# Kernel tuning notes

Measured on AMD Instinct MI355X. Metric: run time of the kernel, lower is better.

Reference implementation:

```python
import jax, jax.numpy as jnp
import numpy as np

B = 1024       # repertoires (batch)
TCR = 100      # instances (TCRs) per repertoire
FEAT = 15      # feature_num (conv in_channels)
AA = 24        # aa_num (sequence length)
KS = [2, 3, 4, 5, 6, 7]
FN = [3, 3, 3, 2, 2, 1]
NINP = 14      # sum(FN)
EPS = 1e-5     # BatchNorm eps


def sparsemax(z):
    # z: (B, K); sparsemax along axis 1 (Martins & Astudillo 2016)
    K = z.shape[1]
    zs = -jnp.sort(-z, axis=1)               # descending sort
    cs = jnp.cumsum(zs, axis=1)
    k = jnp.arange(1, K + 1, dtype=z.dtype)
    support = 1.0 + k * zs > cs              # (B, K) bool
    ksel = jnp.sum(support, axis=1, keepdims=True).astype(jnp.int32)  # support size
    tau = (jnp.take_along_axis(cs, ksel - 1, axis=1) - 1.0) / ksel.astype(z.dtype)
    return jnp.maximum(z - tau, 0.0)


def setup_inputs() -> dict:
    key = jax.random.key(0)
    ks = jax.random.split(key, 12)
    inp = {"x": jax.random.normal(ks[0], (B, TCR, FEAT, AA), dtype=jnp.float32)}
    for i, (h, f) in enumerate(zip(KS, FN)):
        inp[f"cw{i}"] = jax.random.normal(ks[1 + i], (f, FEAT, h), dtype=jnp.float32) * 0.1
        inp[f"cb{i}"] = jnp.zeros((f,), dtype=jnp.float32)
    inp["fc1_w"] = jax.random.normal(ks[7], (NINP, NINP), dtype=jnp.float32) * 0.2
    inp["fc1_b"] = jnp.zeros((NINP,), dtype=jnp.float32)
    inp["waout_w"] = jax.random.normal(ks[8], (1, NINP), dtype=jnp.float32) * 0.2
    inp["decf_w"] = jax.random.normal(ks[9], (NINP, NINP), dtype=jnp.float32) * 0.2
    inp["decf_b"] = jnp.zeros((NINP,), dtype=jnp.float32)
    inp["bn_g"] = jnp.ones((NINP,), dtype=jnp.float32)
    inp["bn_b"] = jnp.zeros((NINP,), dtype=jnp.float32)
    inp["decs_w"] = jax.random.normal(ks[10], (2, NINP), dtype=jnp.float32) * 0.2
    inp["decs_b"] = jnp.zeros((2,), dtype=jnp.float32)
    return inp


def reference(x, cw0, cb0, cw1, cb1, cw2, cb2, cw3, cb3, cw4, cb4, cw5, cb5,
              fc1_w, fc1_b, waout_w, decf_w, decf_b, bn_g, bn_b, decs_w, decs_b):
    xf = x.reshape(-1, FEAT, AA)  # (B*TCR, 15, 24)
    feats = []
    for w, b in ((cw0, cb0), (cw1, cb1), (cw2, cb2), (cw3, cb3), (cw4, cb4), (cw5, cb5)):
        y = jax.lax.conv_general_dilated(xf, w, (1,), 'VALID',
                                         dimension_numbers=('NCH', 'OIH', 'NCH'))
        y = jax.nn.relu(y + b[None, :, None])
        feats.append(jnp.max(y, axis=-1))  # AdaptiveMaxPool1d(1): global max over length
    out = jnp.concatenate(feats, axis=1).reshape(-1, TCR, NINP)  # (B, TCR, 14)
    # fclayer1 + dropout(eval=identity) + relu; applied per-instance so the
    # torch (TCR, B, .) transpose is equivalent to working in (B, TCR, .)
    h = jax.nn.relu(out @ fc1_w.T + fc1_b)                       # (B, TCR, 14)
    attw = sparsemax(h @ waout_w[0])                             # (B, TCR)
    pooled = jnp.einsum('bt,btd->bd', attw, h)                   # bmm(attw[:,None,:], h)
    z = pooled @ decf_w.T + decf_b                               # decoder_f
    mu = jnp.mean(z, axis=0)                                     # BatchNorm1d (batch stats)
    var = jnp.var(z, axis=0)
    z = jax.nn.relu((z - mu) / jnp.sqrt(var + EPS) * bn_g + bn_b)
    logits = z @ decs_w.T + decs_b                               # decoder_s -> (B, 2)
    return logits, attw
```

## Files before the change

### kernel.cpp

```cpp
#include <hip/hip_runtime.h>

typedef unsigned int  u32;
typedef unsigned short u16;

__device__ __forceinline__ float bf2f(u16 u){
    return __uint_as_float(((u32)u) << 16);
}
__device__ __forceinline__ float lo16(u32 v){ return __uint_as_float(v << 16); }
__device__ __forceinline__ float hi16(u32 v){ return __uint_as_float(v & 0xffff0000u); }
__device__ __forceinline__ u16 f2bf(float f){
    u32 x = __float_as_uint(f);
    x += 0x7fffu + ((x >> 16) & 1u);
    return (u16)(x >> 16);
}
__device__ __forceinline__ float ldany(const void* p, int i, bool bf){
    return bf ? bf2f(((const u16*)p)[i]) : ((const float*)p)[i];
}

#define B_      1024
#define TCR_    100
#define NINST   (B_*TCR_)

#define OFF_WCH    0
#define OFF_CB     840
#define OFF_FC1W   854
#define OFF_FC1B   1050
#define OFF_WA     1064
#define OFF_DECFW  1078
#define OFF_DECFB  1274
#define OFF_BNG    1288
#define OFF_BNB    1302
#define OFF_DECSW  1316
#define OFF_DECSB  1344

__global__ __launch_bounds__(256) void k_pack(
    const void* cw0, const void* cb0, const void* cw1, const void* cb1,
    const void* cw2, const void* cb2, const void* cw3, const void* cb3,
    const void* cw4, const void* cb4, const void* cw5, const void* cb5,
    const void* fc1_w, const void* fc1_b, const void* waout,
    const void* decf_w, const void* decf_b,
    const void* bn_g, const void* bn_b,
    const void* decs_w, const void* decs_b,
    float* __restrict__ wsP)
{
    const int tid = threadIdx.x;
    const bool bf = (((const u16*)bn_g)[0] == 0x3F80u);

    for (int widx = tid; widx < 840; widx += 256){
        float val; int dst;
        if (widx < 90)      { int e = widx;       int c=e/6,  rr=e-c*6,  ff=rr/2, j=rr-ff*2; val=ldany(cw0,(ff*15+c)*2+j,bf); dst=c*56+ 0+ff*2+j; }
        else if (widx < 225){ int e = widx - 90;  int c=e/9,  rr=e-c*9,  ff=rr/3, j=rr-ff*3; val=ldany(cw1,(ff*15+c)*3+j,bf); dst=c*56+ 6+ff*3+j; }
        else if (widx < 405){ int e = widx - 225; int c=e/12, rr=e-c*12, ff=rr/4, j=rr-ff*4; val=ldany(cw2,(ff*15+c)*4+j,bf); dst=c*56+15+ff*4+j; }
        else if (widx < 555){ int e = widx - 405; int c=e/10, rr=e-c*10, ff=rr/5, j=rr-ff*5; val=ldany(cw3,(ff*15+c)*5+j,bf); dst=c*56+27+ff*5+j; }
        else if (widx < 735){ int e = widx - 555; int c=e/12, rr=e-c*12, ff=rr/6, j=rr-ff*6; val=ldany(cw4,(ff*15+c)*6+j,bf); dst=c*56+37+ff*6+j; }
        else                { int e = widx - 735; int c=e/7,  j=e-c*7;                        val=ldany(cw5,c*7+j,bf);        dst=c*56+49+j; }
        wsP[OFF_WCH + dst] = val;
    }
    for (int i = tid; i < 14; i += 256){
        float bv;
        if (i < 3)       bv = ldany(cb0, i, bf);
        else if (i < 6)  bv = ldany(cb1, i - 3, bf);
        else if (i < 9)  bv = ldany(cb2, i - 6, bf);
        else if (i < 11) bv = ldany(cb3, i - 9, bf);
        else if (i < 13) bv = ldany(cb4, i - 11, bf);
        else             bv = ldany(cb5, 0, bf);
        wsP[OFF_CB    + i] = bv;
        wsP[OFF_FC1B  + i] = ldany(fc1_b,  i, bf);
        wsP[OFF_WA    + i] = ldany(waout,  i, bf);
        wsP[OFF_DECFB + i] = ldany(decf_b, i, bf);
        wsP[OFF_BNG   + i] = ldany(bn_g,   i, bf);
        wsP[OFF_BNB   + i] = ldany(bn_b,   i, bf);
    }
    for (int i = tid; i < 196; i += 256){
        wsP[OFF_FC1W  + i] = ldany(fc1_w,  i, bf);
        wsP[OFF_DECFW + i] = ldany(decf_w, i, bf);
    }
    for (int i = tid; i < 28; i += 256) wsP[OFF_DECSW + i] = ldany(decs_w, i, bf);
    for (int i = tid; i < 2;  i += 256) wsP[OFF_DECSB + i] = ldany(decs_b, i, bf);
}

template<int H, int F, int GOFF>
__device__ __forceinline__ void acc_ch(float (&acc)[F][17 - H], const float* xr,
                                       const float* __restrict__ wch){
    float wv[F * H];
    #pragma unroll
    for (int k = 0; k < F * H; ++k) wv[k] = wch[GOFF + k];
    #pragma unroll
    for (int ff = 0; ff < F; ++ff)
        #pragma unroll
        for (int i = 0; i < 17 - H; ++i)
            #pragma unroll
            for (int j = 0; j < H; ++j)
                acc[ff][i] = fmaf(wv[ff * H + j], xr[i + j], acc[ff][i]);
}

template<int H, int F, int OF>
__device__ __forceinline__ void pair_max(float (&acc)[F][17 - H],
                                         const float* __restrict__ wsP, float* feats){
    #pragma unroll
    for (int ff = 0; ff < F; ++ff){
        float m = acc[ff][0];
        #pragma unroll
        for (int i = 1; i < 17 - H; ++i) m = fmaxf(m, acc[ff][i]);
        m = fmaxf(m, __shfl_xor(m, 1));
        feats[OF + ff] = fmaxf(m + wsP[OFF_CB + OF + ff], 0.0f);
    }
}

template<bool BF>
__device__ __forceinline__ void unpack16(const uint4* buf, float* xr){
    if (BF){
        #pragma unroll
        for (int i = 0; i < 2; ++i){
            u32 w0 = buf[i].x, w1 = buf[i].y, w2 = buf[i].z, w3 = buf[i].w;
            xr[i*8+0] = lo16(w0); xr[i*8+1] = hi16(w0);
            xr[i*8+2] = lo16(w1); xr[i*8+3] = hi16(w1);
            xr[i*8+4] = lo16(w2); xr[i*8+5] = hi16(w2);
            xr[i*8+6] = lo16(w3); xr[i*8+7] = hi16(w3);
        }
    } else {
        #pragma unroll
        for (int i = 0; i < 4; ++i){
            xr[i*4+0] = __uint_as_float(buf[i].x);
            xr[i*4+1] = __uint_as_float(buf[i].y);
            xr[i*4+2] = __uint_as_float(buf[i].z);
            xr[i*4+3] = __uint_as_float(buf[i].w);
        }
    }
}

template<bool BF>
__device__ __forceinline__ void conv_body(const void* __restrict__ x,
                                          const float* __restrict__ wsP,
                                          float* __restrict__ hbufT,
                                          float* __restrict__ sbuf){
    constexpr int NB = BF ? 2 : 4;
    constexpr int CS = BF ? 48 : 96;
    const int tid   = threadIdx.x;
    const int tpart = tid & 1;
    const int inst  = blockIdx.x * 128 + (tid >> 1);
    const char* xb  = (const char*)x + (size_t)inst * (BF ? 720 : 1440)
                                     + tpart * (BF ? 16 : 32);

    float a2[3][15], a3[3][14], a4[3][13], a5[2][12], a6[2][11], a7[1][10];
    #pragma unroll
    for (int f = 0; f < 3; ++f){
        #pragma unroll
        for (int i = 0; i < 15; ++i) a2[f][i] = 0.0f;
        #pragma unroll
        for (int i = 0; i < 14; ++i) a3[f][i] = 0.0f;
        #pragma unroll
        for (int i = 0; i < 13; ++i) a4[f][i] = 0.0f;
    }
    #pragma unroll
    for (int f = 0; f < 2; ++f){
        #pragma unroll
        for (int i = 0; i < 12; ++i) a5[f][i] = 0.0f;
        #pragma unroll
        for (int i = 0; i < 11; ++i) a6[f][i] = 0.0f;
    }
    #pragma unroll
    for (int i = 0; i < 10; ++i) a7[0][i] = 0.0f;

    uint4 cur[NB];
    {
        const uint4* p = (const uint4*)xb;
        #pragma unroll
        for (int i = 0; i < NB; ++i) cur[i] = p[i];
    }
    #pragma unroll 1
    for (int c = 0; c < 15; ++c){
        uint4 nxt[NB];
        int cn = (c < 14) ? (c + 1) : 14;
        const uint4* pn = (const uint4*)(xb + cn * CS);
        #pragma unroll
        for (int i = 0; i < NB; ++i) nxt[i] = pn[i];

        float xr[16];
        unpack16<BF>(cur, xr);
        const float* wch = wsP + OFF_WCH + c * 56;
        acc_ch<2,3, 0>(a2, xr, wch);
        acc_ch<3,3, 6>(a3, xr, wch);
        acc_ch<4,3,15>(a4, xr, wch);
        acc_ch<5,2,27>(a5, xr, wch);
        acc_ch<6,2,37>(a6, xr, wch);
        acc_ch<7,1,49>(a7, xr, wch);

        #pragma unroll
        for (int i = 0; i < NB; ++i) cur[i] = nxt[i];
    }

    float feats[14];
    pair_max<2,3, 0>(a2, wsP, feats);
    pair_max<3,3, 3>(a3, wsP, feats);
    pair_max<4,3, 6>(a4, wsP, feats);
    pair_max<5,2, 9>(a5, wsP, feats);
    pair_max<6,2,11>(a6, wsP, feats);
    pair_max<7,1,13>(a7, wsP, feats);

    float hv[14];
    #pragma unroll
    for (int i = 0; i < 14; ++i){
        float a = wsP[OFF_FC1B + i];
        #pragma unroll
        for (int j = 0; j < 14; ++j) a = fmaf(feats[j], wsP[OFF_FC1W + i * 14 + j], a);
        hv[i] = fmaxf(a, 0.0f);
    }
    float sc = 0.0f;
    #pragma unroll
    for (int i = 0; i < 14; ++i) sc = fmaf(hv[i], wsP[OFF_WA + i], sc);

    if (tpart == 0){
        #pragma unroll
        for (int d = 0; d < 14; ++d) hbufT[d * NINST + inst] = hv[d];
        sbuf[inst] = sc;
    }
}

__global__ __launch_bounds__(256) void k_conv(
    const void* __restrict__ x, const float* __restrict__ wsP,
    const void* __restrict__ dt,
    float* __restrict__ hbufT, float* __restrict__ sbuf)
{
    const bool bf = (((const u16*)dt)[0] == 0x3F80u);
    if (bf) conv_body<true >(x, wsP, hbufT, sbuf);
    else    conv_body<false>(x, wsP, hbufT, sbuf);
}

__global__ __launch_bounds__(64) void k_sparse(
    const float* __restrict__ hbufT, const float* __restrict__ sbuf,
    const float* __restrict__ wsP, const void* __restrict__ dt,
    float* __restrict__ zbuf, void* __restrict__ d_out)
{
    const int b    = blockIdx.x;
    const int lane = threadIdx.x;
    const bool bf  = (((const u16*)dt)[0] == 0x3F80u);
    const bool has2 = lane < (TCR_ - 64);

    float z0 = sbuf[b * TCR_ + lane];
    float z1 = has2 ? sbuf[b * TCR_ + 64 + lane] : -1e30f;

    float m = fmaxf(z0, z1);
    #pragma unroll
    for (int o = 32; o; o >>= 1) m = fmaxf(m, __shfl_xor(m, o));

    float lo = m - 1.0f, hi = m;
    for (int it = 0; it < 32; ++it){
        float mid = 0.5f * (lo + hi);
        float s = fmaxf(z0 - mid, 0.0f) + fmaxf(z1 - mid, 0.0f);
        #pragma unroll
        for (int o = 32; o; o >>= 1) s += __shfl_xor(s, o);
        if (s >= 1.0f) lo = mid; else hi = mid;
    }
    float tau = 0.5f * (lo + hi);
    float a0 = fmaxf(z0 - tau, 0.0f);
    float a1 = fmaxf(z1 - tau, 0.0f);

    if (bf){
        u16* aw = (u16*)d_out + 2048;
        aw[b * TCR_ + lane] = f2bf(a0);
        if (has2) aw[b * TCR_ + 64 + lane] = f2bf(a1);
    } else {
        float* aw = (float*)d_out + 2048;
        aw[b * TCR_ + lane] = a0;
        if (has2) aw[b * TCR_ + 64 + lane] = a1;
    }

    float ap[14];
    #pragma unroll
    for (int d = 0; d < 14; ++d){
        float v = a0 * hbufT[d * NINST + b * TCR_ + lane];
        if (has2) v += a1 * hbufT[d * NINST + b * TCR_ + 64 + lane];
        #pragma unroll
        for (int o = 32; o; o >>= 1) v += __shfl_xor(v, o);
        ap[d] = v;
    }
    if (lane < 14){
        float zv = wsP[OFF_DECFB + lane];
        #pragma unroll
        for (int j = 0; j < 14; ++j) zv = fmaf(ap[j], wsP[OFF_DECFW + lane * 14 + j], zv);
        zbuf[b * 14 + lane] = zv;
    }
}

__global__ __launch_bounds__(256) void k_bn(
    const float* __restrict__ zbuf, const float* __restrict__ wsP,
    const void* __restrict__ dt, void* __restrict__ d_out)
{
    __shared__ float part[4][28];
    __shared__ float red[28];
    const int tid  = threadIdx.x;
    const int lane = tid & 63;
    const int w    = tid >> 6;
    const bool bf  = (((const u16*)dt)[0] == 0x3F80u);

    float z[4][14];
    #pragma unroll
    for (int r = 0; r < 4; ++r)
        #pragma unroll
        for (int d = 0; d < 14; ++d) z[r][d] = zbuf[(tid + 256 * r) * 14 + d];

    #pragma unroll
    for (int d = 0; d < 14; ++d){
        float s = 0.0f, q = 0.0f;
        #pragma unroll
        for (int r = 0; r < 4; ++r){ s += z[r][d]; q += z[r][d] * z[r][d]; }
        #pragma unroll
        for (int o = 32; o; o >>= 1){ s += __shfl_xor(s, o); q += __shfl_xor(q, o); }
        if (lane == 0){ part[w][d] = s; part[w][14 + d] = q; }
    }
    __syncthreads();
    if (tid < 28) red[tid] = part[0][tid] + part[1][tid] + part[2][tid] + part[3][tid];
    __syncthreads();

    float mu[14], rs[14];
    #pragma unroll
    for (int d = 0; d < 14; ++d){
        mu[d] = red[d] * (1.0f / 1024.0f);
        float var = red[14 + d] * (1.0f / 1024.0f) - mu[d] * mu[d];
        rs[d] = rsqrtf(var + 1e-5f);
    }
    #pragma unroll
    for (int r = 0; r < 4; ++r){
        float zn[14];
        #pragma unroll
        for (int d = 0; d < 14; ++d)
            zn[d] = fmaxf((z[r][d] - mu[d]) * rs[d] * wsP[OFF_BNG + d] + wsP[OFF_BNB + d], 0.0f);
        #pragma unroll
        for (int c = 0; c < 2; ++c){
            float a = wsP[OFF_DECSB + c];
            #pragma unroll
            for (int d = 0; d < 14; ++d) a = fmaf(zn[d], wsP[OFF_DECSW + c * 14 + d], a);
            if (bf) ((u16*)d_out)[(tid + 256 * r) * 2 + c] = f2bf(a);
            else    ((float*)d_out)[(tid + 256 * r) * 2 + c] = a;
        }
    }
}

extern "C" void kernel_launch(void* const* d_in, const int* in_sizes, int n_in,
                              void* d_out, int out_size, void* d_ws, size_t ws_size,
                              hipStream_t stream)
{
    (void)in_sizes; (void)n_in; (void)out_size; (void)ws_size;
    const void* x     = d_in[0];
    const void* bn_g  = d_in[18];

    float* wsP   = (float*)d_ws;
    float* hbufT = wsP + 2048;
    float* sbuf  = hbufT + (size_t)14 * NINST;
    float* zbuf  = sbuf + NINST;

    k_pack<<<1, 256, 0, stream>>>(
        d_in[1], d_in[2], d_in[3], d_in[4], d_in[5], d_in[6],
        d_in[7], d_in[8], d_in[9], d_in[10], d_in[11], d_in[12],
        d_in[13], d_in[14], d_in[15], d_in[16], d_in[17],
        d_in[18], d_in[19], d_in[20], d_in[21], wsP);
    k_conv<<<NINST / 128, 256, 0, stream>>>(x, wsP, bn_g, hbufT, sbuf);
    k_sparse<<<B_, 64, 0, stream>>>(hbufT, sbuf, wsP, bn_g, zbuf, d_out);
    k_bn<<<1, 256, 0, stream>>>(zbuf, wsP, bn_g, d_out);
}
```

Before: 298.3 us.

## Recast bf16 conv as Toeplitz MFMA GEMM and restructure fp32 conv per-lane

```diff
diff --git a/kernel.cpp b/kernel.cpp
--- a/kernel.cpp
+++ b/kernel.cpp
@@ -2,12 +2,12 @@
 
 typedef unsigned int  u32;
 typedef unsigned short u16;
+typedef __attribute__((ext_vector_type(8))) short short8;
+typedef __attribute__((ext_vector_type(4))) float f32x4;
 
 __device__ __forceinline__ float bf2f(u16 u){
     return __uint_as_float(((u32)u) << 16);
 }
-__device__ __forceinline__ float lo16(u32 v){ return __uint_as_float(v << 16); }
-__device__ __forceinline__ float hi16(u32 v){ return __uint_as_float(v & 0xffff0000u); }
 __device__ __forceinline__ u16 f2bf(float f){
     u32 x = __float_as_uint(f);
     x += 0x7fffu + ((x >> 16) & 1u);
@@ -20,6 +20,9 @@
 #define B_      1024
 #define TCR_    100
 #define NINST   (B_*TCR_)
+#define NT      21
+#define KS      12
+#define K2      384
 
 #define OFF_WCH    0
 #define OFF_CB     840
@@ -32,6 +35,7 @@
 #define OFF_BNB    1302
 #define OFF_DECSW  1316
 #define OFF_DECSB  1344
+#define OFF_HBUF   66560
 
 __global__ __launch_bounds__(256) void k_pack(
     const void* cw0, const void* cb0, const void* cw1, const void* cb1,
@@ -46,157 +50,177 @@
     const int tid = threadIdx.x;
     const bool bf = (((const u16*)bn_g)[0] == 0x3F80u);
 
-    for (int widx = tid; widx < 840; widx += 256){
-        float val; int dst;
-        if (widx < 90)      { int e = widx;       int c=e/6,  rr=e-c*6,  ff=rr/2, j=rr-ff*2; val=ldany(cw0,(ff*15+c)*2+j,bf); dst=c*56+ 0+ff*2+j; }
-        else if (widx < 225){ int e = widx - 90;  int c=e/9,  rr=e-c*9,  ff=rr/3, j=rr-ff*3; val=ldany(cw1,(ff*15+c)*3+j,bf); dst=c*56+ 6+ff*3+j; }
-        else if (widx < 405){ int e = widx - 225; int c=e/12, rr=e-c*12, ff=rr/4, j=rr-ff*4; val=ldany(cw2,(ff*15+c)*4+j,bf); dst=c*56+15+ff*4+j; }
-        else if (widx < 555){ int e = widx - 405; int c=e/10, rr=e-c*10, ff=rr/5, j=rr-ff*5; val=ldany(cw3,(ff*15+c)*5+j,bf); dst=c*56+27+ff*5+j; }
-        else if (widx < 735){ int e = widx - 555; int c=e/12, rr=e-c*12, ff=rr/6, j=rr-ff*6; val=ldany(cw4,(ff*15+c)*6+j,bf); dst=c*56+37+ff*6+j; }
-        else                { int e = widx - 735; int c=e/7,  j=e-c*7;                        val=ldany(cw5,c*7+j,bf);        dst=c*56+49+j; }
-        wsP[OFF_WCH + dst] = val;
-    }
-    for (int i = tid; i < 14; i += 256){
-        float bv;
-        if (i < 3)       bv = ldany(cb0, i, bf);
-        else if (i < 6)  bv = ldany(cb1, i - 3, bf);
-        else if (i < 9)  bv = ldany(cb2, i - 6, bf);
-        else if (i < 11) bv = ldany(cb3, i - 9, bf);
-        else if (i < 13) bv = ldany(cb4, i - 11, bf);
-        else             bv = ldany(cb5, 0, bf);
-        wsP[OFF_CB    + i] = bv;
-        wsP[OFF_FC1B  + i] = ldany(fc1_b,  i, bf);
-        wsP[OFF_WA    + i] = ldany(waout,  i, bf);
-        wsP[OFF_DECFB + i] = ldany(decf_b, i, bf);
-        wsP[OFF_BNG   + i] = ldany(bn_g,   i, bf);
-        wsP[OFF_BNB   + i] = ldany(bn_b,   i, bf);
-    }
-    for (int i = tid; i < 196; i += 256){
-        wsP[OFF_FC1W  + i] = ldany(fc1_w,  i, bf);
-        wsP[OFF_DECFW + i] = ldany(decf_w, i, bf);
-    }
-    for (int i = tid; i < 28; i += 256) wsP[OFF_DECSW + i] = ldany(decs_w, i, bf);
-    for (int i = tid; i < 2;  i += 256) wsP[OFF_DECSB + i] = ldany(decs_b, i, bf);
-}
-
-template<int H, int F, int GOFF>
-__device__ __forceinline__ void acc_ch(float (&acc)[F][17 - H], const float* xr,
-                                       const float* __restrict__ wch){
-    float wv[F * H];
-    #pragma unroll
-    for (int k = 0; k < F * H; ++k) wv[k] = wch[GOFF + k];
+    if (blockIdx.x == 0){
+        for (int widx = tid; widx < 840; widx += 256){
+            float val; int dst;
+            if (widx < 90)      { int e = widx;       int c=e/6,  rr=e-c*6,  ff=rr/2, j=rr-ff*2; val=ldany(cw0,(ff*15+c)*2+j,bf); dst=c*56+ 0+ff*2+j; }
+            else if (widx < 225){ int e = widx - 90;  int c=e/9,  rr=e-c*9,  ff=rr/3, j=rr-ff*3; val=ldany(cw1,(ff*15+c)*3+j,bf); dst=c*56+ 6+ff*3+j; }
+            else if (widx < 405){ int e = widx - 225; int c=e/12, rr=e-c*12, ff=rr/4, j=rr-ff*4; val=ldany(cw2,(ff*15+c)*4+j,bf); dst=c*56+15+ff*4+j; }
+            else if (widx < 555){ int e = widx - 405; int c=e/10, rr=e-c*10, ff=rr/5, j=rr-ff*5; val=ldany(cw3,(ff*15+c)*5+j,bf); dst=c*56+27+ff*5+j; }
+            else if (widx < 735){ int e = widx - 555; int c=e/12, rr=e-c*12, ff=rr/6, j=rr-ff*6; val=ldany(cw4,(ff*15+c)*6+j,bf); dst=c*56+37+ff*6+j; }
+            else                { int e = widx - 735; int c=e/7,  j=e-c*7;                        val=ldany(cw5,c*7+j,bf);        dst=c*56+49+j; }
+            wsP[OFF_WCH + dst] = val;
+        }
+        for (int i = tid; i < 14; i += 256){
+            float bv;
+            if (i < 3)       bv = ldany(cb0, i, bf);
+            else if (i < 6)  bv = ldany(cb1, i - 3, bf);
+            else if (i < 9)  bv = ldany(cb2, i - 6, bf);
+            else if (i < 11) bv = ldany(cb3, i - 9, bf);
+            else if (i < 13) bv = ldany(cb4, i - 11, bf);
+            else             bv = ldany(cb5, 0, bf);
+            wsP[OFF_CB    + i] = bv;
+            wsP[OFF_FC1B  + i] = ldany(fc1_b,  i, bf);
+            wsP[OFF_WA    + i] = ldany(waout,  i, bf);
+            wsP[OFF_DECFB + i] = ldany(decf_b, i, bf);
+            wsP[OFF_BNG   + i] = ldany(bn_g,   i, bf);
+            wsP[OFF_BNB   + i] = ldany(bn_b,   i, bf);
+        }
+        for (int i = tid; i < 196; i += 256){
+            wsP[OFF_FC1W  + i] = ldany(fc1_w,  i, bf);
+            wsP[OFF_DECFW + i] = ldany(decf_w, i, bf);
+        }
+        for (int i = tid; i < 28; i += 256) wsP[OFF_DECSW + i] = ldany(decs_w, i, bf);
+        for (int i = tid; i < 2;  i += 256) wsP[OFF_DECSB + i] = ldany(decs_b, i, bf);
+    }
+
+    u16* wt = (u16*)(wsP + 2048);
+    const int gstride = gridDim.x * 256;
+    for (int i = blockIdx.x * 256 + tid; i < 336 * K2; i += gstride){
+        int n = i / K2, k = i - n * K2;
+        int gff = n / 24, t = n - gff * 24;
+        int H = 2 + (gff>=3) + (gff>=6) + (gff>=9) + (gff>=11) + (gff>=13);
+        int limit = 25 - H;
+        float val = 0.0f;
+        if (k < 360 && t < limit){
+            int c = k / 24, u = k - c * 24;
+            int j = u - t;
+            if (j >= 0 && j < H){
+                if (gff < 3)       val = ldany(cw0, ((gff  )*15+c)*2+j, bf);
+                else if (gff < 6)  val = ldany(cw1, ((gff-3)*15+c)*3+j, bf);
+                else if (gff < 9)  val = ldany(cw2, ((gff-6)*15+c)*4+j, bf);
+                else if (gff < 11) val = ldany(cw3, ((gff-9)*15+c)*5+j, bf);
+                else if (gff < 13) val = ldany(cw4, ((gff-11)*15+c)*6+j, bf);
+                else               val = ldany(cw5, (c)*7+j, bf);
+            }
+        }
+        wt[(size_t)n * K2 + k] = f2bf(val);
+    }
+}
+
+template<int H, int F, int GOFF, int OF>
+__device__ __forceinline__ void f32_group(const float* __restrict__ xrow,
+                                          const float* __restrict__ wsP,
+                                          float* feats){
+    float acc[F][25 - H];
     #pragma unroll
     for (int ff = 0; ff < F; ++ff)
         #pragma unroll
-        for (int i = 0; i < 17 - H; ++i)
-            #pragma unroll
-            for (int j = 0; j < H; ++j)
-                acc[ff][i] = fmaf(wv[ff * H + j], xr[i + j], acc[ff][i]);
-}
-
-template<int H, int F, int OF>
-__device__ __forceinline__ void pair_max(float (&acc)[F][17 - H],
-                                         const float* __restrict__ wsP, float* feats){
+        for (int t = 0; t < 25 - H; ++t) acc[ff][t] = 0.0f;
+    for (int c = 0; c < 15; ++c){
+        float xr[24];
+        const float4* p = (const float4*)(xrow + c * 24);
+        #pragma unroll
+        for (int i = 0; i < 6; ++i){
+            float4 v = p[i];
+            xr[i*4+0] = v.x; xr[i*4+1] = v.y; xr[i*4+2] = v.z; xr[i*4+3] = v.w;
+        }
+        const float* wc = wsP + OFF_WCH + c * 56 + GOFF;
+        #pragma unroll
+        for (int ff = 0; ff < F; ++ff)
+            #pragma unroll
+            for (int t = 0; t < 25 - H; ++t)
+                #pragma unroll
+                for (int j = 0; j < H; ++j)
+                    acc[ff][t] = fmaf(wc[ff * H + j], xr[t + j], acc[ff][t]);
+    }
     #pragma unroll
     for (int ff = 0; ff < F; ++ff){
         float m = acc[ff][0];
         #pragma unroll
-        for (int i = 1; i < 17 - H; ++i) m = fmaxf(m, acc[ff][i]);
-        m = fmaxf(m, __shfl_xor(m, 1));
-        feats[OF + ff] = fmaxf(m + wsP[OFF_CB + OF + ff], 0.0f);
-    }
-}
-
-template<bool BF>
-__device__ __forceinline__ void unpack16(const uint4* buf, float* xr){
-    if (BF){
-        #pragma unroll
-        for (int i = 0; i < 2; ++i){
-            u32 w0 = buf[i].x, w1 = buf[i].y, w2 = buf[i].z, w3 = buf[i].w;
-            xr[i*8+0] = lo16(w0); xr[i*8+1] = hi16(w0);
-            xr[i*8+2] = lo16(w1); xr[i*8+3] = hi16(w1);
-            xr[i*8+4] = lo16(w2); xr[i*8+5] = hi16(w2);
-            xr[i*8+6] = lo16(w3); xr[i*8+7] = hi16(w3);
+        for (int t = 1; t < 25 - H; ++t) m = fmaxf(m, acc[ff][t]);
+        feats[OF + ff] = m;
+    }
+}
+
+__global__ __launch_bounds__(64, 2) void k_conv(
+    const void* __restrict__ x, const float* __restrict__ wsP,
+    const u16* __restrict__ wt, const void* __restrict__ dt,
+    float* __restrict__ hbufT, float* __restrict__ sbuf)
+{
+    __shared__ float pool[64][43];
+    const int lane = threadIdx.x;
+    const bool bf  = (((const u16*)dt)[0] == 0x3F80u);
+    const int instbase = blockIdx.x * 64;
+
+    float feats[14];
+
+    if (bf){
+        const int col  = lane & 15;
+        const int quad = lane >> 4;
+
+        short8 A[4][KS];
+        #pragma unroll
+        for (int ms = 0; ms < 4; ++ms){
+            const u16* xrow = (const u16*)x + (size_t)(instbase + ms * 16 + col) * 360;
+            #pragma unroll
+            for (int ks = 0; ks < KS; ++ks){
+                int k0 = ks * 32 + quad * 8;
+                if (k0 >= 360) k0 = 0;
+                A[ms][ks] = *(const short8*)(xrow + k0);
+            }
+        }
+
+        #pragma unroll 1
+        for (int nt = 0; nt < NT; ++nt){
+            f32x4 C[4];
+            #pragma unroll
+            for (int ms = 0; ms < 4; ++ms) C[ms] = (f32x4){0.f, 0.f, 0.f, 0.f};
+
+            const u16* wrow = wt + (size_t)(nt * 16 + col) * K2 + quad * 8;
+            #pragma unroll
+            for (int ks = 0; ks < KS; ++ks){
+                short8 Bf = *(const short8*)(wrow + ks * 32);
+                #pragma unroll
+                for (int ms = 0; ms < 4; ++ms)
+                    C[ms] = __builtin_amdgcn_mfma_f32_16x16x32_bf16(A[ms][ks], Bf, C[ms], 0, 0, 0);
+            }
+
+            int n = nt * 16 + col;
+            int g = (n * 2731) >> 16;
+            int pos = n - g * 24;
+            int limit = 23 - (g>=3) - (g>=6) - (g>=9) - (g>=11) - (g>=13);
+            bool valid = pos < limit;
+            int h = nt * 2 + (col >> 3);
+            #pragma unroll
+            for (int ms = 0; ms < 4; ++ms)
+                #pragma unroll
+                for (int r = 0; r < 4; ++r){
+                    float v = valid ? C[ms][r] : -3.0e38f;
+                    v = fmaxf(v, __shfl_xor(v, 1));
+                    v = fmaxf(v, __shfl_xor(v, 2));
+                    v = fmaxf(v, __shfl_xor(v, 4));
+                    if ((col & 7) == 0)
+                        pool[ms * 16 + quad * 4 + r][h] = v;
+                }
+        }
+        #pragma unroll
+        for (int g = 0; g < 14; ++g){
+            float m = fmaxf(fmaxf(pool[lane][3*g], pool[lane][3*g+1]), pool[lane][3*g+2]);
+            feats[g] = fmaxf(m + wsP[OFF_CB + g], 0.0f);
         }
     } else {
-        #pragma unroll
-        for (int i = 0; i < 4; ++i){
-            xr[i*4+0] = __uint_as_float(buf[i].x);
-            xr[i*4+1] = __uint_as_float(buf[i].y);
-            xr[i*4+2] = __uint_as_float(buf[i].z);
-            xr[i*4+3] = __uint_as_float(buf[i].w);
-        }
-    }
-}
-
-template<bool BF>
-__device__ __forceinline__ void conv_body(const void* __restrict__ x,
-                                          const float* __restrict__ wsP,
-                                          float* __restrict__ hbufT,
-                                          float* __restrict__ sbuf){
-    constexpr int NB = BF ? 2 : 4;
-    constexpr int CS = BF ? 48 : 96;
-    const int tid   = threadIdx.x;
-    const int tpart = tid & 1;
-    const int inst  = blockIdx.x * 128 + (tid >> 1);
-    const char* xb  = (const char*)x + (size_t)inst * (BF ? 720 : 1440)
-                                     + tpart * (BF ? 16 : 32);
-
-    float a2[3][15], a3[3][14], a4[3][13], a5[2][12], a6[2][11], a7[1][10];
-    #pragma unroll
-    for (int f = 0; f < 3; ++f){
-        #pragma unroll
-        for (int i = 0; i < 15; ++i) a2[f][i] = 0.0f;
-        #pragma unroll
-        for (int i = 0; i < 14; ++i) a3[f][i] = 0.0f;
-        #pragma unroll
-        for (int i = 0; i < 13; ++i) a4[f][i] = 0.0f;
-    }
-    #pragma unroll
-    for (int f = 0; f < 2; ++f){
-        #pragma unroll
-        for (int i = 0; i < 12; ++i) a5[f][i] = 0.0f;
-        #pragma unroll
-        for (int i = 0; i < 11; ++i) a6[f][i] = 0.0f;
-    }
-    #pragma unroll
-    for (int i = 0; i < 10; ++i) a7[0][i] = 0.0f;
-
-    uint4 cur[NB];
-    {
-        const uint4* p = (const uint4*)xb;
-        #pragma unroll
-        for (int i = 0; i < NB; ++i) cur[i] = p[i];
-    }
-    #pragma unroll 1
-    for (int c = 0; c < 15; ++c){
-        uint4 nxt[NB];
-        int cn = (c < 14) ? (c + 1) : 14;
-        const uint4* pn = (const uint4*)(xb + cn * CS);
-        #pragma unroll
-        for (int i = 0; i < NB; ++i) nxt[i] = pn[i];
-
-        float xr[16];
-        unpack16<BF>(cur, xr);
-        const float* wch = wsP + OFF_WCH + c * 56;
-        acc_ch<2,3, 0>(a2, xr, wch);
-        acc_ch<3,3, 6>(a3, xr, wch);
-        acc_ch<4,3,15>(a4, xr, wch);
-        acc_ch<5,2,27>(a5, xr, wch);
-        acc_ch<6,2,37>(a6, xr, wch);
-        acc_ch<7,1,49>(a7, xr, wch);
-
-        #pragma unroll
-        for (int i = 0; i < NB; ++i) cur[i] = nxt[i];
-    }
-
-    float feats[14];
-    pair_max<2,3, 0>(a2, wsP, feats);
-    pair_max<3,3, 3>(a3, wsP, feats);
-    pair_max<4,3, 6>(a4, wsP, feats);
-    pair_max<5,2, 9>(a5, wsP, feats);
-    pair_max<6,2,11>(a6, wsP, feats);
-    pair_max<7,1,13>(a7, wsP, feats);
+        const float* xrow = (const float*)x + (size_t)(instbase + lane) * 360;
+        f32_group<2,3, 0, 0>(xrow, wsP, feats);
+        f32_group<3,3, 6, 3>(xrow, wsP, feats);
+        f32_group<4,3,15, 6>(xrow, wsP, feats);
+        f32_group<5,2,27, 9>(xrow, wsP, feats);
+        f32_group<6,2,37,11>(xrow, wsP, feats);
+        f32_group<7,1,49,13>(xrow, wsP, feats);
+        #pragma unroll
+        for (int g = 0; g < 14; ++g)
+            feats[g] = fmaxf(feats[g] + wsP[OFF_CB + g], 0.0f);
+    }
 
     float hv[14];
     #pragma unroll
@@ -210,21 +234,10 @@
     #pragma unroll
     for (int i = 0; i < 14; ++i) sc = fmaf(hv[i], wsP[OFF_WA + i], sc);
 
-    if (tpart == 0){
-        #pragma unroll
-        for (int d = 0; d < 14; ++d) hbufT[d * NINST + inst] = hv[d];
-        sbuf[inst] = sc;
-    }
-}
-
-__global__ __launch_bounds__(256) void k_conv(
-    const void* __restrict__ x, const float* __restrict__ wsP,
-    const void* __restrict__ dt,
-    float* __restrict__ hbufT, float* __restrict__ sbuf)
-{
-    const bool bf = (((const u16*)dt)[0] == 0x3F80u);
-    if (bf) conv_body<true >(x, wsP, hbufT, sbuf);
-    else    conv_body<false>(x, wsP, hbufT, sbuf);
+    const int inst = instbase + lane;
+    #pragma unroll
+    for (int d = 0; d < 14; ++d) hbufT[d * NINST + inst] = hv[d];
+    sbuf[inst] = sc;
 }
 
 __global__ __launch_bounds__(64) void k_sparse(
@@ -346,16 +359,17 @@
     const void* bn_g  = d_in[18];
 
     float* wsP   = (float*)d_ws;
-    float* hbufT = wsP + 2048;
+    u16*   wt    = (u16*)(wsP + 2048);
+    float* hbufT = wsP + OFF_HBUF;
     float* sbuf  = hbufT + (size_t)14 * NINST;
     float* zbuf  = sbuf + NINST;
 
-    k_pack<<<1, 256, 0, stream>>>(
+    k_pack<<<64, 256, 0, stream>>>(
         d_in[1], d_in[2], d_in[3], d_in[4], d_in[5], d_in[6],
         d_in[7], d_in[8], d_in[9], d_in[10], d_in[11], d_in[12],
         d_in[13], d_in[14], d_in[15], d_in[16], d_in[17],
         d_in[18], d_in[19], d_in[20], d_in[21], wsP);
-    k_conv<<<NINST / 128, 256, 0, stream>>>(x, wsP, bn_g, hbufT, sbuf);
+    k_conv<<<NINST / 64, 64, 0, stream>>>(x, wsP, wt, bn_g, hbufT, sbuf);
     k_sparse<<<B_, 64, 0, stream>>>(hbufT, sbuf, wsP, bn_g, zbuf, d_out);
     k_bn<<<1, 256, 0, stream>>>(zbuf, wsP, bn_g, d_out);
 }
```

Measured after the change: 439.7 us. +47.4%, slower.
